# Performance work log

Hardware: AMD Instinct MI355X
Metric: run time of the kernel (lower is better)

The kernel has to match this reference:

```python
import jax, jax.numpy as jnp
import numpy as np

LN_EPS = 1e-5


def conv2d(x, w, b, stride, pad):
    # x: NCHW, w: OIHW
    y = jax.lax.conv_general_dilated(
        x, w, (stride, stride), [(pad, pad), (pad, pad)],
        dimension_numbers=("NCHW", "OIHW", "NCHW"))
    return y + b[None, :, None, None]


def gdn(x, gamma, beta):
    # y_c = x_c / sqrt(beta_c + sum_j gamma_cj * x_j^2)  (1x1 conv on x^2)
    norm = jnp.einsum("bchw,dc->bdhw", x * x, gamma) + beta[None, :, None, None]
    return x / jnp.sqrt(norm)


def layernorm(x, w, b):
    mu = jnp.mean(x, axis=-1, keepdims=True)
    var = jnp.var(x, axis=-1, keepdims=True)
    return (x - mu) / jnp.sqrt(var + LN_EPS) * w + b


def setup_inputs() -> dict:
    key = jax.random.key(0)
    ks = jax.random.split(key, 16)
    r = lambda i, shape: (jax.random.normal(ks[i], shape) * 0.02).astype(jnp.float32)
    N, M, K, D = 128, 192, 192, 128
    return {
        "x_p": jax.random.normal(ks[0], (4, 16, 3, 64, 64), jnp.float32),
        "y_g": jax.random.normal(ks[1], (64, K, 32), jnp.float32),
        "conv1_w": r(2, (N, 3, 5, 5)), "conv1_b": jnp.zeros((N,), jnp.float32),
        "gamma1": (0.1 * jnp.eye(N) + 1e-3).astype(jnp.float32), "beta1": jnp.ones((N,), jnp.float32),
        "conv2_w": r(3, (N, N, 5, 5)), "conv2_b": jnp.zeros((N,), jnp.float32),
        "gamma2": (0.1 * jnp.eye(N) + 1e-3).astype(jnp.float32), "beta2": jnp.ones((N,), jnp.float32),
        "conv3_w": r(4, (M, N, 3, 3)), "conv3_b": jnp.zeros((M,), jnp.float32),
        "ln_q_w": jnp.ones((M,), jnp.float32), "ln_q_b": jnp.zeros((M,), jnp.float32),
        "ln_kv_w": jnp.ones((K,), jnp.float32), "ln_kv_b": jnp.zeros((K,), jnp.float32),
        "ln_out_w": jnp.ones((M,), jnp.float32), "ln_out_b": jnp.zeros((M,), jnp.float32),
        "Wq": r(5, (D, M)), "Wk": r(6, (D, K)), "v_w": r(7, (1, D)),
        "Wv": r(8, (M, K)), "out_w": r(9, (M, M)), "out_b": jnp.zeros((M,), jnp.float32),
    }


def reference(x_p, y_g, conv1_w, conv1_b, gamma1, beta1, conv2_w, conv2_b,
              gamma2, beta2, conv3_w, conv3_b, ln_q_w, ln_q_b, ln_kv_w, ln_kv_b,
              ln_out_w, ln_out_b, Wq, Wk, v_w, Wv, out_w, out_b):
    B, P, C, Hp, Wp = x_p.shape
    x = x_p.reshape(B * P, C, Hp, Wp)
    # local encoder: conv s2 -> GDN -> conv s2 -> GDN -> conv s1 k3
    x = gdn(conv2d(x, conv1_w, conv1_b, 2, 2), gamma1, beta1)
    x = gdn(conv2d(x, conv2_w, conv2_b, 2, 2), gamma2, beta2)
    y_local = conv2d(x, conv3_w, conv3_b, 1, 1)          # (BP, M, h, w)
    BP, M, h, w = y_local.shape
    q = y_local.reshape(BP, M, h * w).transpose(0, 2, 1)  # (BP, Tq, M)
    kv = y_g.reshape(BP, y_g.shape[1], -1).transpose(0, 2, 1)  # (BP, Tk, K)
    q = layernorm(q, ln_q_w, ln_q_b)
    kv = layernorm(kv, ln_kv_w, ln_kv_b)
    # Bahdanau additive attention
    q_proj = jnp.einsum("bqm,dm->bqd", q, Wq)            # (BP, Tq, D)
    k_proj = jnp.einsum("bkc,dc->bkd", kv, Wk)           # (BP, Tk, D)
    energy = jnp.einsum("bqkd,d->bqk",
                        jnp.tanh(q_proj[:, :, None, :] + k_proj[:, None, :, :]),
                        v_w[0])                           # (BP, Tq, Tk)
    alpha = jax.nn.softmax(energy, axis=-1)
    v_proj = jnp.einsum("bkc,mc->bkm", kv, Wv)           # (BP, Tk, M)
    context = jnp.einsum("bqk,bkm->bqm", alpha, v_proj)
    context = jnp.einsum("bqm,nm->bqn", context, out_w) + out_b
    fused = layernorm(q + context, ln_out_w, ln_out_b)
    return fused.transpose(0, 2, 1).reshape(BP, M, h, w)
```

## Files before the change

kernel.cpp:

```cpp
#include <hip/hip_runtime.h>
#include <cstddef>
#include <cstdint>


typedef __bf16 bf16x8 __attribute__((ext_vector_type(8)));
typedef float floatx4 __attribute__((ext_vector_type(4)));
typedef unsigned short ushortT;
typedef unsigned short ushort8v __attribute__((ext_vector_type(8)));

#if __has_builtin(__builtin_amdgcn_exp2f)
#define EXP2F(x) __builtin_amdgcn_exp2f(x)
#else
#define EXP2F(x) exp2f(x)
#endif
#if __has_builtin(__builtin_amdgcn_rcpf)
#define RCPF(x) __builtin_amdgcn_rcpf(x)
#else
#define RCPF(x) (1.f / (x))
#endif

__device__ __forceinline__ ushortT f2bf(float f) {
  unsigned u = __builtin_bit_cast(unsigned, f);
  unsigned r = (u + 0x7FFFu + ((u >> 16) & 1u)) >> 16;
  return (ushortT)r;
}
__device__ __forceinline__ float bf2f(ushortT u) {
  return __builtin_bit_cast(float, ((unsigned)u) << 16);
}

static constexpr size_t OFF_T1BF = 0;
static constexpr size_t OFF_X2BF = 4194304;
static constexpr size_t OFF_T2BF = 8388608;
static constexpr size_t OFF_X3BF = 9437184;
static constexpr size_t OFF_QRAW = 10485760;
static constexpr size_t OFF_QLNB = 16777216;
static constexpr size_t OFF_KVB  = 18350080;
static constexpr size_t OFF_QP   = 18546688;
static constexpr size_t OFF_KP   = 20643840;
static constexpr size_t OFF_VP   = 20905984;
static constexpr size_t OFF_WBQ  = 21299200;
static constexpr size_t OFF_WBK  = 21311488;
static constexpr size_t OFF_WBV  = 21323776;
static constexpr size_t OFF_WBO  = 21342208;
static constexpr size_t OFF_CTXB = 21360640;
static constexpr size_t OFF_WT2  = 26079232;
static constexpr size_t OFF_WT3  = 26284032;
static constexpr size_t OFF_WC1  = 26394624;
static constexpr size_t OFF_GB1  = 26406912;
static constexpr size_t OFF_GB2  = 26415104;

__device__ __constant__ int d_TWI2[4][9] = {{ 0, 2, 4,10,12,14,20,22,24},
                                            { 1, 3,11,13,21,23, 0, 0, 0},
                                            { 5, 7, 9,15,17,19, 0, 0, 0},
                                            { 6, 8,16,18, 0, 0, 0, 0, 0}};
__device__ __constant__ int d_NT2[4] = {9, 6, 6, 4};

__device__ void dev_convw3(const float* w, ushortT* wt, int mode, int total,
                           int idx) {
  if (idx >= total) return;
  int j    = idx & 7;
  int om   = (idx >> 3) & 63;
  int kg   = (idx >> 9) & 3;
  int slab = idx >> 11;
  int mt, s, tap, T;
  if (mode == 0) {
    int ph;
    if (slab < 72) ph = 0; else if (slab < 120) ph = 1;
    else if (slab < 168) ph = 2; else ph = 3;
    const int st[4] = {0, 72, 120, 168};
    const int ns[4] = {36, 24, 24, 16};
    int rel = slab - st[ph];
    mt = rel / ns[ph]; s = rel % ns[ph];
    tap = d_TWI2[ph][s >> 2]; T = 25;
  } else {
    mt = slab / 36; s = slab % 36; tap = s >> 2; T = 9;
  }
  int cc = s & 3;
  int c  = cc * 32 + kg * 8 + j;
  int oc = mt * 64 + om;
  wt[idx] = f2bf(w[(size_t)(oc * 128 + c) * T + tap]);
}

__device__ void dev_convw1(const float* w, ushortT* wt, int idx) {
  if (idx >= 20480) return;
  int k    = idx & 31;
  int oc   = (idx >> 5) & 127;
  int slab = idx >> 12;
  int ph, i;
  if (slab < 2) { ph = 0; i = slab; } else { ph = slab - 1; i = 0; }
  int kg = k >> 3, jj = k & 7;
  int tidx = i * 8 + jj;
  float val = 0.f;
  if (kg < 3 && tidx < d_NT2[ph]) {
    int tap = d_TWI2[ph][tidx];
    val = w[(size_t)(oc * 3 + kg) * 25 + tap];
  }
  wt[idx] = f2bf(val);
}

__device__ void dev_wcast(const float* w, ushortT* wb, int total, float scale,
                          int idx) {
  if (idx < total) wb[idx] = f2bf(w[idx] * scale);
}

__global__ __launch_bounds__(256) void prep_kernel(
    const float* __restrict__ conv2_w, ushortT* __restrict__ wt2,
    const float* __restrict__ conv3_w, ushortT* __restrict__ wt3,
    const float* __restrict__ conv1_w, ushortT* __restrict__ wc1,
    const float* __restrict__ Wq, ushortT* __restrict__ wbq,
    const float* __restrict__ Wk, ushortT* __restrict__ wbk,
    const float* __restrict__ Wv, ushortT* __restrict__ wbv,
    const float* __restrict__ out_w, ushortT* __restrict__ wbo,
    const float* __restrict__ gamma1, ushortT* __restrict__ gb1,
    const float* __restrict__ gamma2, ushortT* __restrict__ gb2) {
  constexpr float C2LE = 2.88539008177792681f;
  int blk = blockIdx.x, tid = threadIdx.x;
  if (blk < 1600)      dev_convw3(conv2_w, wt2, 0, 409600, blk * 256 + tid);
  else if (blk < 2464) dev_convw3(conv3_w, wt3, 1, 221184, (blk - 1600) * 256 + tid);
  else if (blk < 2544) dev_convw1(conv1_w, wc1, (blk - 2464) * 256 + tid);
  else if (blk < 2640) dev_wcast(Wq, wbq, 24576, C2LE, (blk - 2544) * 256 + tid);
  else if (blk < 2736) dev_wcast(Wk, wbk, 24576, C2LE, (blk - 2640) * 256 + tid);
  else if (blk < 2880) dev_wcast(Wv, wbv, 36864, 1.f, (blk - 2736) * 256 + tid);
  else if (blk < 3024) dev_wcast(out_w, wbo, 36864, 1.f, (blk - 2880) * 256 + tid);
  else if (blk < 3088) dev_wcast(gamma1, gb1, 16384, 1.f, (blk - 3024) * 256 + tid);
  else                 dev_wcast(gamma2, gb2, 16384, 1.f, (blk - 3088) * 256 + tid);
}

__global__ __launch_bounds__(256, 1) void conv1_mfma_kernel(
    const float* __restrict__ x, const ushortT* __restrict__ wc1,
    const float* __restrict__ bias, ushortT* __restrict__ outb) {
  int b  = blockIdx.x >> 2;
  int yg = blockIdx.x & 3;
  int y0 = yg * 8;

  int wave = threadIdx.x >> 6;
  int lane = threadIdx.x & 63;
  int ln15 = lane & 15;
  int kg   = lane >> 4;
  int tid  = threadIdx.x;

  __shared__ ushortT simg[4680];
  __shared__ ushortT sA[5 * 128 * 40];

  for (int j = tid; j < 2340; j += 256) ((unsigned*)simg)[j] = 0u;
  __syncthreads();

  int ihBase = 2 * y0 - 2;
  const float* xb = x + (size_t)b * 3 * 4096;
  for (int j = tid; j < 960; j += 256) {
    int q = j & 15;
    int rr = j >> 4;
    int c = rr / 20, ihl = rr % 20;
    int ih = ihBase + ihl;
    if (ih >= 0 && ih < 64) {
      float4 v = *(const float4*)&xb[c * 4096 + ih * 64 + q * 4];
      int pr = ih & 1, u = ih >> 1;
      int lr = u - y0 + 1;
      int base0 = ((pr * 2 + 0) * 3 + c) * 360 + lr * 36;
      int base1 = ((pr * 2 + 1) * 3 + c) * 360 + lr * 36;
      simg[base0 + 2 * q + 1] = f2bf(v.x);
      simg[base1 + 2 * q + 1] = f2bf(v.y);
      simg[base0 + 2 * q + 2] = f2bf(v.z);
      simg[base1 + 2 * q + 2] = f2bf(v.w);
    }
  }
  for (int j = tid; j < 2560; j += 256) {
    int chunk = j & 3, row = j >> 2;
    uint4 v = *(const uint4*)&wc1[row * 32 + chunk * 8];
    *(uint4*)&sA[row * 40 + chunk * 8] = v;
  }
  __syncthreads();

  constexpr int TDR[4][9] = {{-1,-1,-1, 0, 0, 0, 1, 1, 1},
                             {-1,-1, 0, 0, 1, 1, 0, 0, 0},
                             {-1,-1,-1, 0, 0, 0, 0, 0, 0},
                             {-1,-1, 0, 0, 0, 0, 0, 0, 0}};
  constexpr int TDC[4][9] = {{-1, 0, 1,-1, 0, 1,-1, 0, 1},
                             {-1, 0,-1, 0,-1, 0, 0, 0, 0},
                             {-1, 0, 1,-1, 0, 1, 0, 0, 0},
                             {-1, 0,-1, 0, 0, 0, 0, 0, 0}};
  constexpr int NT[4]  = {9, 6, 6, 4};
  constexpr int NM[4]  = {2, 1, 1, 1};
  constexpr int SB[4]  = {0, 2, 3, 4};

  ushort8v Bf[4][5];
  #pragma unroll
  for (int ntl = 0; ntl < 4; ++ntl) {
    int ntg = wave * 4 + ntl;
    int yloc = ntg >> 1;
    int xx = (ntg & 1) * 16 + ln15;
    int lbase = (yloc + 1) * 36 + xx + 1 + kg * 360;
    #pragma unroll
    for (int ph = 0; ph < 4; ++ph) {
      int pbase = ph * 1080 + lbase;
      #pragma unroll
      for (int i = 0; i < 2; ++i) {
        if (i < NM[ph]) {
          ushort8v bv;
          #pragma unroll
          for (int j = 0; j < 8; ++j) {
            int tidx = i * 8 + j;
            if (tidx >= NT[ph]) tidx = 0;
            int off = TDR[ph][tidx] * 36 + TDC[ph][tidx];
            bv[j] = simg[pbase + off];
          }
          Bf[ntl][SB[ph] + i] = bv;
        }
      }
    }
  }

  #pragma unroll
  for (int m = 0; m < 8; ++m) {
    bf16x8 Af[5];
    #pragma unroll
    for (int s = 0; s < 5; ++s)
      Af[s] = *(const bf16x8*)&sA[(s * 128 + m * 16 + ln15) * 40 + kg * 8];
    int oc0 = m * 16 + kg * 4;
    float4 bv = *(const float4*)&bias[oc0];
    #pragma unroll
    for (int ntl = 0; ntl < 4; ++ntl) {
      floatx4 acc = (floatx4)0.f;
      #pragma unroll
      for (int s = 0; s < 5; ++s)
        acc = __builtin_amdgcn_mfma_f32_16x16x32_bf16(
            Af[s], __builtin_bit_cast(bf16x8, Bf[ntl][s]), acc, 0, 0, 0);
      int ntg = wave * 4 + ntl;
      int y = y0 + (ntg >> 1);
      int xx = (ntg & 1) * 16 + ln15;
      int p = y * 32 + xx;
      ushort4 o4 = {f2bf(acc[0] + bv.x), f2bf(acc[1] + bv.y),
                    f2bf(acc[2] + bv.z), f2bf(acc[3] + bv.w)};
      *(ushort4*)&outb[((size_t)b * 1024 + p) * 128 + oc0] = o4;
    }
  }
}

__global__ __launch_bounds__(256) void gdn_mfma_kernel(
    const ushortT* __restrict__ xbf, const ushortT* __restrict__ gb,
    const float* __restrict__ beta, ushortT* __restrict__ ybf,
    int HW, int nPixTiles, int isSplit) {
  int pt = blockIdx.x % nPixTiles;
  int b  = blockIdx.x / nPixTiles;
  int px0 = pt * 64;
  int tid = threadIdx.x;
  int wave = tid >> 6, lane = tid & 63, ln15 = lane & 15, kg = lane >> 4;

  __shared__ ushortT sG[128 * 136];
  __shared__ ushortT sX[64 * 136];

  for (int j = tid; j < 2048; j += 256) {
    int row = j >> 4, ch = j & 15;
    *(uint4*)&sG[row * 136 + ch * 8] = *(const uint4*)&gb[row * 128 + ch * 8];
  }
  for (int j = tid; j < 1024; j += 256) {
    int row = j >> 4, ch = j & 15;
    ushort8v xv = *(const ushort8v*)&xbf[((size_t)(b * HW + px0 + row)) * 128 + ch * 8];
    ushort8v sq;
    #pragma unroll
    for (int r = 0; r < 8; ++r) {
      float f = bf2f(xv[r]);
      sq[r] = f2bf(f * f);
    }
    *(ushort8v*)&sX[row * 136 + ch * 8] = sq;
  }
  __syncthreads();

  floatx4 acc[2][4];
  #pragma unroll
  for (int mi = 0; mi < 2; ++mi)
    #pragma unroll
    for (int nt = 0; nt < 4; ++nt) acc[mi][nt] = (floatx4)0.f;

  #pragma unroll
  for (int k0 = 0; k0 < 128; k0 += 32) {
    bf16x8 a0 = *(const bf16x8*)&sG[(wave * 32 + ln15) * 136 + k0 + kg * 8];
    bf16x8 a1 = *(const bf16x8*)&sG[(wave * 32 + 16 + ln15) * 136 + k0 + kg * 8];
    #pragma unroll
    for (int nt = 0; nt < 4; ++nt) {
      bf16x8 bb = *(const bf16x8*)&sX[(nt * 16 + ln15) * 136 + k0 + kg * 8];
      acc[0][nt] = __builtin_amdgcn_mfma_f32_16x16x32_bf16(a0, bb, acc[0][nt], 0, 0, 0);
      acc[1][nt] = __builtin_amdgcn_mfma_f32_16x16x32_bf16(a1, bb, acc[1][nt], 0, 0, 0);
    }
  }

  #pragma unroll
  for (int mi = 0; mi < 2; ++mi) {
    int d0 = wave * 32 + mi * 16 + kg * 4;
    float4 bt = *(const float4*)&beta[d0];
    #pragma unroll
    for (int nt = 0; nt < 4; ++nt) {
      int p = px0 + nt * 16 + ln15;
      ushort4 x4 = *(const ushort4*)&xbf[((size_t)(b * HW + p)) * 128 + d0];
      ushort4 o4;
      o4.x = f2bf(bf2f(x4.x) * rsqrtf(acc[mi][nt][0] + bt.x));
      o4.y = f2bf(bf2f(x4.y) * rsqrtf(acc[mi][nt][1] + bt.y));
      o4.z = f2bf(bf2f(x4.z) * rsqrtf(acc[mi][nt][2] + bt.z));
      o4.w = f2bf(bf2f(x4.w) * rsqrtf(acc[mi][nt][3] + bt.w));
      size_t dst;
      if (isSplit) {
        int h = p >> 5, w5 = p & 31;
        int ph = ((h & 1) << 1) | (w5 & 1);
        dst = (((size_t)b * 4 + ph) * 256 + (h >> 1) * 16 + (w5 >> 1)) * 128 + d0;
      } else {
        dst = ((size_t)b * 256 + p) * 128 + d0;
      }
      *(ushort4*)&ybf[dst] = o4;
    }
  }
}

template<int MODE>
__global__ __launch_bounds__(256, 2) void conv_mfma_kernel(
    const ushortT* __restrict__ X,
    const ushortT* __restrict__ Wt,
    const float* __restrict__ bias,
    ushortT* __restrict__ outb) {
  constexpr int OC  = (MODE == 0) ? 128 : 192;
  constexpr int NMT = OC / 64;
  constexpr int NPH = (MODE == 0) ? 4 : 1;

  int b   = blockIdx.x / (NMT * 4);
  int rem = blockIdx.x % (NMT * 4);
  int mt  = rem >> 2;
  int rs  = rem & 3;
  int r0  = rs * 4;

  int wave = threadIdx.x >> 6;
  int lane = threadIdx.x & 63;
  int ln15 = lane & 15;
  int kg   = lane >> 4;

  __shared__ ushortT simg[6 * 18 * 136];

  floatx4 acc[4];
  #pragma unroll
  for (int m = 0; m < 4; ++m) acc[m] = (floatx4)0.f;

  constexpr int NS2[4]      = {36, 24, 24, 16};
  constexpr int PHSTART2[4] = {0, 72, 120, 168};
  constexpr int TDR_2[4][9] = {{-1,-1,-1, 0, 0, 0, 1, 1, 1},
                               {-1,-1, 0, 0, 1, 1, 0, 0, 0},
                               {-1,-1,-1, 0, 0, 0, 0, 0, 0},
                               {-1,-1, 0, 0, 0, 0, 0, 0, 0}};
  constexpr int TDC_2[4][9] = {{-1, 0, 1,-1, 0, 1,-1, 0, 1},
                               {-1, 0,-1, 0,-1, 0, 0, 0, 0},
                               {-1, 0, 1,-1, 0, 1, 0, 0, 0},
                               {-1, 0,-1, 0, 0, 0, 0, 0, 0}};
  constexpr int TDR_3[9] = {-1,-1,-1, 0, 0, 0, 1, 1, 1};
  constexpr int TDC_3[9] = {-1, 0, 1,-1, 0, 1,-1, 0, 1};

  const int aoff = kg * 512 + ln15 * 8;
  uint4 apf[8][4];

  #pragma unroll
  for (int ph = 0; ph < NPH; ++ph) {
    const int NS = (MODE == 0) ? NS2[ph] : 36;
    const int slabBase = (MODE == 0) ? (PHSTART2[ph] + mt * NS2[ph]) : (mt * 36);
    const ushortT* wp0 = Wt + (size_t)slabBase * 2048 + aoff;

    __syncthreads();
    const ushortT* Xb = X + (((size_t)b * NPH + ph) * 256) * 128;
    for (int idx = threadIdx.x; idx < 1728; idx += 256) {
      int chunk = idx & 15;
      int pix = idx >> 4;
      int row = pix / 18, colm = pix - row * 18;
      int i = r0 - 1 + row, j = colm - 1;
      uint4 v = {0u, 0u, 0u, 0u};
      if (i >= 0 && i < 16 && j >= 0 && j < 16)
        v = *(const uint4*)(Xb + ((size_t)(i * 16 + j)) * 128 + chunk * 8);
      *(uint4*)&simg[(row * 18 + colm) * 136 + chunk * 8] = v;
    }
    #pragma unroll
    for (int jj = 0; jj < 8; ++jj)
      if (jj < NS) {
        #pragma unroll
        for (int m = 0; m < 4; ++m)
          apf[jj][m] = *(const uint4*)(wp0 + (size_t)jj * 2048 + m * 128);
      }
    __syncthreads();

    #pragma unroll
    for (int s0 = 0; s0 < NS; s0 += 8) {
      #pragma unroll
      for (int jj = 0; jj < 8; ++jj) {
        int s = s0 + jj;
        if (s < NS) {
          bf16x8 acur[4];
          #pragma unroll
          for (int m = 0; m < 4; ++m) acur[m] = __builtin_bit_cast(bf16x8, apf[jj][m]);
          int sp = s + 8;
          if (sp < NS) {
            #pragma unroll
            for (int m = 0; m < 4; ++m)
              apf[jj][m] = *(const uint4*)(wp0 + (size_t)sp * 2048 + m * 128);
          }
          int t  = s >> 2;
          int c0 = (s & 3) * 32;
          int dr = (MODE == 0) ? TDR_2[ph][t] : TDR_3[t];
          int dc = (MODE == 0) ? TDC_2[ph][t] : TDC_3[t];
          int lrow = wave + dr + 1;
          int lcol = ln15 + dc + 1;
          bf16x8 bfr = *(const bf16x8*)&simg[(lrow * 18 + lcol) * 136 + c0 + kg * 8];
          #pragma unroll
          for (int m = 0; m < 4; ++m)
            acc[m] = __builtin_amdgcn_mfma_f32_16x16x32_bf16(acur[m], bfr, acc[m], 0, 0, 0);
        }
      }
    }
  }

  #pragma unroll
  for (int m = 0; m < 4; ++m) {
    int mg = mt * 64 + m * 16 + kg * 4;
    float4 bv = *(const float4*)&bias[mg];
    int r = r0 + wave;
    int p = r * 16 + ln15;
    ushort4 o4 = {f2bf(acc[m][0] + bv.x), f2bf(acc[m][1] + bv.y),
                  f2bf(acc[m][2] + bv.z), f2bf(acc[m][3] + bv.w)};
    *(ushort4*)&outb[((size_t)b * 256 + p) * OC + mg] = o4;
  }
}

__device__ __forceinline__ void gemm_body(
    const ushortT* A, const ushortT* Bm, ushortT* C,
    int N, int r0, int n0, int tid) {
  __shared__ ushortT sA[128 * 196];
  __shared__ ushortT sB[64 * 196];
  for (int j = tid; j < 3072; j += 256) {
    int row = j / 24, ch = j % 24;
    *(ushort8v*)&sA[row * 196 + ch * 8] = *(const ushort8v*)&A[(size_t)(r0 + row) * 192 + ch * 8];
  }
  for (int j = tid; j < 1536; j += 256) {
    int row = j / 24, ch = j % 24;
    *(ushort8v*)&sB[row * 196 + ch * 8] = *(const ushort8v*)&Bm[(size_t)(n0 + row) * 192 + ch * 8];
  }
  __syncthreads();
  int wave = tid >> 6, lane = tid & 63, ln15 = lane & 15, kg = lane >> 4;
  floatx4 acc[2][4];
  #pragma unroll
  for (int m = 0; m < 2; ++m)
    #pragma unroll
    for (int n = 0; n < 4; ++n) acc[m][n] = (floatx4)0.f;

  #pragma unroll
  for (int k0 = 0; k0 < 192; k0 += 32) {
    bf16x8 afr[2];
    #pragma unroll
    for (int m = 0; m < 2; ++m)
      afr[m] = *(const bf16x8*)&sA[(wave * 32 + m * 16 + ln15) * 196 + k0 + kg * 8];
    #pragma unroll
    for (int n = 0; n < 4; ++n) {
      bf16x8 bfr = *(const bf16x8*)&sB[(n * 16 + ln15) * 196 + k0 + kg * 8];
      acc[0][n] = __builtin_amdgcn_mfma_f32_16x16x32_bf16(afr[0], bfr, acc[0][n], 0, 0, 0);
      acc[1][n] = __builtin_amdgcn_mfma_f32_16x16x32_bf16(afr[1], bfr, acc[1][n], 0, 0, 0);
    }
  }
  #pragma unroll
  for (int n = 0; n < 4; ++n) {
    int col = n0 + n * 16 + ln15;
    #pragma unroll
    for (int m = 0; m < 2; ++m) {
      int rowb = r0 + wave * 32 + m * 16 + kg * 4;
      #pragma unroll
      for (int r = 0; r < 4; ++r)
        C[(size_t)(rowb + r) * N + col] = f2bf(acc[m][n][r]);
    }
  }
}

__global__ __launch_bounds__(256) void gemm_qkv_kernel(
    const ushortT* __restrict__ qlnb, const ushortT* __restrict__ kvb,
    const ushortT* __restrict__ wbq, const ushortT* __restrict__ wbk,
    const ushortT* __restrict__ wbv,
    ushortT* __restrict__ qpb, ushortT* __restrict__ kpb,
    ushortT* __restrict__ vpb) {
  int blk = blockIdx.x, tid = threadIdx.x;
  if (blk < 256) {
    gemm_body(qlnb, wbq, qpb, 128, (blk >> 1) * 128, (blk & 1) * 64, tid);
  } else if (blk < 288) {
    int k = blk - 256;
    gemm_body(kvb, wbk, kpb, 128, (k >> 1) * 128, (k & 1) * 64, tid);
  } else {
    int k = blk - 288;
    gemm_body(kvb, wbv, vpb, 192, (k / 3) * 128, (k % 3) * 64, tid);
  }
}

__global__ __launch_bounds__(256) void ln_all_kernel(
    const ushortT* __restrict__ qrawb, const float* __restrict__ qw,
    const float* __restrict__ qb, ushortT* __restrict__ qlnb,
    const float* __restrict__ yg, const float* __restrict__ kw,
    const float* __restrict__ kb, ushortT* __restrict__ kvb) {
  int lane = threadIdx.x & 63;
  if (blockIdx.x < 4096) {
    int row = blockIdx.x * 4 + (threadIdx.x >> 6);
    const ushortT* xr = qrawb + (size_t)row * 192;
    float v0 = bf2f(xr[lane]), v1 = bf2f(xr[lane + 64]), v2 = bf2f(xr[lane + 128]);
    float s = v0 + v1 + v2;
    float s2 = v0 * v0 + v1 * v1 + v2 * v2;
    #pragma unroll
    for (int off = 32; off; off >>= 1) { s += __shfl_xor(s, off); s2 += __shfl_xor(s2, off); }
    float mean = s * (1.f / 192.f);
    float var = s2 * (1.f / 192.f) - mean * mean;
    float inv = rsqrtf(var + 1e-5f);
    ushortT* ybr = qlnb + (size_t)row * 192;
    ybr[lane]       = f2bf((v0 - mean) * inv * qw[lane]       + qb[lane]);
    ybr[lane + 64]  = f2bf((v1 - mean) * inv * qw[lane + 64]  + qb[lane + 64]);
    ybr[lane + 128] = f2bf((v2 - mean) * inv * qw[lane + 128] + qb[lane + 128]);
  } else {
    int row = (blockIdx.x - 4096) * 4 + (threadIdx.x >> 6);
    int b = row >> 5, t = row & 31;
    const float* src = yg + (size_t)b * 6144 + t;
    float v0 = src[(size_t)lane * 32];
    float v1 = src[(size_t)(lane + 64) * 32];
    float v2 = src[(size_t)(lane + 128) * 32];
    float s = v0 + v1 + v2;
    float s2 = v0 * v0 + v1 * v1 + v2 * v2;
    #pragma unroll
    for (int off = 32; off; off >>= 1) { s += __shfl_xor(s, off); s2 += __shfl_xor(s2, off); }
    float mean = s * (1.f / 192.f);
    float var = s2 * (1.f / 192.f) - mean * mean;
    float inv = rsqrtf(var + 1e-5f);
    ushortT* yr = kvb + (size_t)row * 192;
    yr[lane]       = f2bf((v0 - mean) * inv * kw[lane]       + kb[lane]);
    yr[lane + 64]  = f2bf((v1 - mean) * inv * kw[lane + 64]  + kb[lane + 64]);
    yr[lane + 128] = f2bf((v2 - mean) * inv * kw[lane + 128] + kb[lane + 128]);
  }
}

__global__ __launch_bounds__(256) void attn_kernel(
    const ushortT* __restrict__ qpb, const ushortT* __restrict__ kpb,
    const ushortT* __restrict__ vpb, const float* __restrict__ vw,
    ushortT* __restrict__ ctxb) {
  int b = blockIdx.x >> 4;
  int q0 = (blockIdx.x & 15) * 16;
  __shared__ float skp[32 * 132];
  __shared__ float sqp[16 * 132];
  __shared__ float svp[32 * 192];
  __shared__ float se[16][33];
  __shared__ float swm[128];
  __shared__ float sS0;
  int tid = threadIdx.x;

  for (int j = tid; j < 512; j += 256) {
    int k = j >> 4, d8 = j & 15;
    ushort8v v = *(const ushort8v*)&kpb[((size_t)(b * 32 + k)) * 128 + d8 * 8];
    #pragma unroll
    for (int r = 0; r < 8; ++r) skp[k * 132 + d8 * 8 + r] = bf2f(v[r]);
  }
  for (int j = tid; j < 256; j += 256) {
    int qq = j >> 4, d8 = j & 15;
    ushort8v v = *(const ushort8v*)&qpb[((size_t)(b * 256 + q0 + qq)) * 128 + d8 * 8];
    #pragma unroll
    for (int r = 0; r < 8; ++r) sqp[qq * 132 + d8 * 8 + r] = bf2f(v[r]);
  }
  for (int j = tid; j < 768; j += 256) {
    int k = j / 24, c8 = j % 24;
    ushort8v v = *(const ushort8v*)&vpb[((size_t)(b * 32 + k)) * 192 + c8 * 8];
    #pragma unroll
    for (int r = 0; r < 8; ++r) svp[k * 192 + c8 * 8 + r] = bf2f(v[r]);
  }
  if (tid < 128) swm[tid] = -2.f * vw[tid];
  if (tid < 64) {
    float s = vw[tid] + vw[tid + 64];
    #pragma unroll
    for (int off = 32; off; off >>= 1) s += __shfl_xor(s, off);
    if (tid == 0) sS0 = s;
  }
  __syncthreads();

  {
    int qq = tid >> 4, kc = tid & 15;
    const float4* q4 = (const float4*)&sqp[qq * 132];
    const float4* ka = (const float4*)&skp[kc * 132];
    const float4* kb = (const float4*)&skp[(kc + 16) * 132];
    const float4* w4 = (const float4*)swm;
    float S0 = sS0;
    float acc0 = S0, acc1 = S0;
    #pragma unroll 8
    for (int dj = 0; dj < 32; ++dj) {
      float4 qv = q4[dj], k0 = ka[dj], k1 = kb[dj], wv = w4[dj];
      acc0 += wv.x * RCPF(EXP2F(qv.x + k0.x) + 1.f);
      acc0 += wv.y * RCPF(EXP2F(qv.y + k0.y) + 1.f);
      acc0 += wv.z * RCPF(EXP2F(qv.z + k0.z) + 1.f);
      acc0 += wv.w * RCPF(EXP2F(qv.w + k0.w) + 1.f);
      acc1 += wv.x * RCPF(EXP2F(qv.x + k1.x) + 1.f);
      acc1 += wv.y * RCPF(EXP2F(qv.y + k1.y) + 1.f);
      acc1 += wv.z * RCPF(EXP2F(qv.z + k1.z) + 1.f);
      acc1 += wv.w * RCPF(EXP2F(qv.w + k1.w) + 1.f);
    }
    se[qq][kc] = acc0;
    se[qq][kc + 16] = acc1;
  }
  __syncthreads();
  if (tid < 16) {
    float mx = -1e30f;
    for (int k = 0; k < 32; ++k) mx = fmaxf(mx, se[tid][k]);
    float s = 0.f;
    for (int k = 0; k < 32; ++k) { float a = __expf(se[tid][k] - mx); se[tid][k] = a; s += a; }
    float invs = 1.f / s;
    for (int k = 0; k < 32; ++k) se[tid][k] *= invs;
  }
  __syncthreads();
  for (int j = tid; j < 768; j += 256) {
    int qq = j / 48, m4 = j % 48;
    const float* al = se[qq];
    float4 a = {0.f, 0.f, 0.f, 0.f};
    #pragma unroll 8
    for (int k = 0; k < 32; ++k) {
      float wk = al[k];
      float4 v = *(const float4*)&svp[k * 192 + m4 * 4];
      a.x += wk * v.x; a.y += wk * v.y; a.z += wk * v.z; a.w += wk * v.w;
    }
    ushort4 o4 = {f2bf(a.x), f2bf(a.y), f2bf(a.z), f2bf(a.w)};
    *(ushort4*)&ctxb[((size_t)(b * 256 + q0 + qq)) * 192 + m4 * 4] = o4;
  }
}

__global__ __launch_bounds__(256) void outproj_ln_kernel(
    const ushortT* __restrict__ ctxb, const ushortT* __restrict__ wbo,
    const float* __restrict__ out_b, const ushortT* __restrict__ qlnb,
    const float* __restrict__ w, const float* __restrict__ bb,
    float* __restrict__ out) {
  int b = blockIdx.x >> 2;
  int t0 = (blockIdx.x & 3) * 64;
  __shared__ float sf[64 * 193];
  int tid = threadIdx.x;
  int wave = tid >> 6, lane = tid & 63, ln15 = lane & 15, kg = lane >> 4;

  const ushortT* Arow = ctxb + ((size_t)(b * 256 + t0)) * 192;

  #pragma unroll
  for (int nc = 0; nc < 3; ++nc) {
    floatx4 acc[4];
    #pragma unroll
    for (int n = 0; n < 4; ++n) acc[n] = (floatx4)0.f;
    #pragma unroll
    for (int k0 = 0; k0 < 192; k0 += 32) {
      bf16x8 afr = *(const bf16x8*)&Arow[((size_t)(wave * 16 + ln15)) * 192 + k0 + kg * 8];
      #pragma unroll
      for (int n = 0; n < 4; ++n) {
        bf16x8 bfr = *(const bf16x8*)&wbo[((size_t)(nc * 64 + n * 16 + ln15)) * 192 + k0 + kg * 8];
        acc[n] = __builtin_amdgcn_mfma_f32_16x16x32_bf16(afr, bfr, acc[n], 0, 0, 0);
      }
    }
    #pragma unroll
    for (int n = 0; n < 4; ++n) {
      int col = nc * 64 + n * 16 + ln15;
      float bv = out_b[col];
      #pragma unroll
      for (int r = 0; r < 4; ++r)
        sf[(wave * 16 + kg * 4 + r) * 193 + col] = acc[n][r] + bv;
    }
  }
  __syncthreads();

  for (int rr = wave; rr < 64; rr += 4) {
    size_t gb = ((size_t)(b * 256 + t0 + rr)) * 192;
    float v0 = sf[rr * 193 + lane]       + bf2f(qlnb[gb + lane]);
    float v1 = sf[rr * 193 + lane + 64]  + bf2f(qlnb[gb + lane + 64]);
    float v2 = sf[rr * 193 + lane + 128] + bf2f(qlnb[gb + lane + 128]);
    float s = v0 + v1 + v2;
    float s2 = v0 * v0 + v1 * v1 + v2 * v2;
    #pragma unroll
    for (int off = 32; off; off >>= 1) { s += __shfl_xor(s, off); s2 += __shfl_xor(s2, off); }
    float mean = s * (1.f / 192.f);
    float var = s2 * (1.f / 192.f) - mean * mean;
    float inv = rsqrtf(var + 1e-5f);
    sf[rr * 193 + lane]       = (v0 - mean) * inv * w[lane]       + bb[lane];
    sf[rr * 193 + lane + 64]  = (v1 - mean) * inv * w[lane + 64]  + bb[lane + 64];
    sf[rr * 193 + lane + 128] = (v2 - mean) * inv * w[lane + 128] + bb[lane + 128];
  }
  __syncthreads();

  for (int j = tid; j < 192 * 16; j += 256) {
    int m = j >> 4, t4 = j & 15;
    float4 o4;
    o4.x = sf[(t4 * 4 + 0) * 193 + m];
    o4.y = sf[(t4 * 4 + 1) * 193 + m];
    o4.z = sf[(t4 * 4 + 2) * 193 + m];
    o4.w = sf[(t4 * 4 + 3) * 193 + m];
    *(float4*)&out[((size_t)(b * 192 + m)) * 256 + t0 + t4 * 4] = o4;
  }
}

extern "C" void kernel_launch(void* const* d_in, const int* in_sizes, int n_in,
                              void* d_out, int out_size, void* d_ws, size_t ws_size,
                              hipStream_t stream) {
  (void)in_sizes; (void)n_in; (void)out_size; (void)ws_size;
  const float* x_p     = (const float*)d_in[0];
  const float* y_g     = (const float*)d_in[1];
  const float* conv1_w = (const float*)d_in[2];
  const float* conv1_b = (const float*)d_in[3];
  const float* gamma1  = (const float*)d_in[4];
  const float* beta1   = (const float*)d_in[5];
  const float* conv2_w = (const float*)d_in[6];
  const float* conv2_b = (const float*)d_in[7];
  const float* gamma2  = (const float*)d_in[8];
  const float* beta2   = (const float*)d_in[9];
  const float* conv3_w = (const float*)d_in[10];
  const float* conv3_b = (const float*)d_in[11];
  const float* ln_q_w  = (const float*)d_in[12];
  const float* ln_q_b  = (const float*)d_in[13];
  const float* ln_kv_w = (const float*)d_in[14];
  const float* ln_kv_b = (const float*)d_in[15];
  const float* ln_out_w= (const float*)d_in[16];
  const float* ln_out_b= (const float*)d_in[17];
  const float* Wq      = (const float*)d_in[18];
  const float* Wk      = (const float*)d_in[19];
  const float* v_w     = (const float*)d_in[20];
  const float* Wv      = (const float*)d_in[21];
  const float* out_w   = (const float*)d_in[22];
  const float* out_b   = (const float*)d_in[23];
  float* out = (float*)d_out;
  float* ws  = (float*)d_ws;

  ushortT* t1bf  = (ushortT*)(ws + OFF_T1BF);
  ushortT* x2bf  = (ushortT*)(ws + OFF_X2BF);
  ushortT* t2bf  = (ushortT*)(ws + OFF_T2BF);
  ushortT* x3bf  = (ushortT*)(ws + OFF_X3BF);
  ushortT* qrawb = (ushortT*)(ws + OFF_QRAW);
  ushortT* qlnb  = (ushortT*)(ws + OFF_QLNB);
  ushortT* kvb   = (ushortT*)(ws + OFF_KVB);
  ushortT* qpb   = (ushortT*)(ws + OFF_QP);
  ushortT* kpb   = (ushortT*)(ws + OFF_KP);
  ushortT* vpb   = (ushortT*)(ws + OFF_VP);
  ushortT* wbq   = (ushortT*)(ws + OFF_WBQ);
  ushortT* wbk   = (ushortT*)(ws + OFF_WBK);
  ushortT* wbv   = (ushortT*)(ws + OFF_WBV);
  ushortT* wbo   = (ushortT*)(ws + OFF_WBO);
  ushortT* ctxb  = (ushortT*)(ws + OFF_CTXB);
  ushortT* wt2   = (ushortT*)(ws + OFF_WT2);
  ushortT* wt3   = (ushortT*)(ws + OFF_WT3);
  ushortT* wc1   = (ushortT*)(ws + OFF_WC1);
  ushortT* gb1   = (ushortT*)(ws + OFF_GB1);
  ushortT* gb2   = (ushortT*)(ws + OFF_GB2);

  prep_kernel<<<3152, 256, 0, stream>>>(conv2_w, wt2, conv3_w, wt3, conv1_w, wc1,
                                        Wq, wbq, Wk, wbk, Wv, wbv, out_w, wbo,
                                        gamma1, gb1, gamma2, gb2);
  conv1_mfma_kernel<<<256, 256, 0, stream>>>(x_p, wc1, conv1_b, t1bf);
  gdn_mfma_kernel<<<1024, 256, 0, stream>>>(t1bf, gb1, beta1, x2bf, 1024, 16, 1);
  conv_mfma_kernel<0><<<512, 256, 0, stream>>>(x2bf, wt2, conv2_b, t2bf);
  gdn_mfma_kernel<<<256, 256, 0, stream>>>(t2bf, gb2, beta2, x3bf, 256, 4, 0);
  conv_mfma_kernel<1><<<768, 256, 0, stream>>>(x3bf, wt3, conv3_b, qrawb);
  ln_all_kernel<<<4608, 256, 0, stream>>>(qrawb, ln_q_w, ln_q_b, qlnb,
                                          y_g, ln_kv_w, ln_kv_b, kvb);
  gemm_qkv_kernel<<<336, 256, 0, stream>>>(qlnb, kvb, wbq, wbk, wbv,
                                           qpb, kpb, vpb);
  attn_kernel<<<1024, 256, 0, stream>>>(qpb, kpb, vpb, v_w, ctxb);
  outproj_ln_kernel<<<256, 256, 0, stream>>>(ctxb, wbo, out_b, qlnb,
                                             ln_out_w, ln_out_b, out);
}
```

Measured before the change: 264.1 us.

## Fuse LayerNorm, QKV projections, attention and output projection into one kernel

Merges four kernels (LN, QKV GEMM, additive attention, outproj+LN) into one per-(batch, 64-token) block kernel that keeps intermediates in shared memory. This removes the global-memory round trips for qln, kv, q/k/v projections and context, plus three launches. The cost is that K/V LN and projections are recomputed by each of the 4 blocks per batch, and only 256 blocks run with large LDS use. The attention energy loop now reads bf16 from LDS instead of fp32, and the q LayerNorm is recomputed at the residual step.

```diff
diff --git a/kernel.cpp b/kernel.cpp
--- a/kernel.cpp
+++ b/kernel.cpp
@@ -33,16 +33,10 @@
 static constexpr size_t OFF_T2BF = 8388608;
 static constexpr size_t OFF_X3BF = 9437184;
 static constexpr size_t OFF_QRAW = 10485760;
-static constexpr size_t OFF_QLNB = 16777216;
-static constexpr size_t OFF_KVB  = 18350080;
-static constexpr size_t OFF_QP   = 18546688;
-static constexpr size_t OFF_KP   = 20643840;
-static constexpr size_t OFF_VP   = 20905984;
 static constexpr size_t OFF_WBQ  = 21299200;
 static constexpr size_t OFF_WBK  = 21311488;
 static constexpr size_t OFF_WBV  = 21323776;
 static constexpr size_t OFF_WBO  = 21342208;
-static constexpr size_t OFF_CTXB = 21360640;
 static constexpr size_t OFF_WT2  = 26079232;
 static constexpr size_t OFF_WT3  = 26284032;
 static constexpr size_t OFF_WC1  = 26394624;
@@ -422,80 +416,37 @@
   }
 }
 
-__device__ __forceinline__ void gemm_body(
-    const ushortT* A, const ushortT* Bm, ushortT* C,
-    int N, int r0, int n0, int tid) {
-  __shared__ ushortT sA[128 * 196];
-  __shared__ ushortT sB[64 * 196];
-  for (int j = tid; j < 3072; j += 256) {
-    int row = j / 24, ch = j % 24;
-    *(ushort8v*)&sA[row * 196 + ch * 8] = *(const ushort8v*)&A[(size_t)(r0 + row) * 192 + ch * 8];
-  }
-  for (int j = tid; j < 1536; j += 256) {
-    int row = j / 24, ch = j % 24;
-    *(ushort8v*)&sB[row * 196 + ch * 8] = *(const ushort8v*)&Bm[(size_t)(n0 + row) * 192 + ch * 8];
-  }
-  __syncthreads();
-  int wave = tid >> 6, lane = tid & 63, ln15 = lane & 15, kg = lane >> 4;
-  floatx4 acc[2][4];
-  #pragma unroll
-  for (int m = 0; m < 2; ++m)
-    #pragma unroll
-    for (int n = 0; n < 4; ++n) acc[m][n] = (floatx4)0.f;
-
-  #pragma unroll
-  for (int k0 = 0; k0 < 192; k0 += 32) {
-    bf16x8 afr[2];
-    #pragma unroll
-    for (int m = 0; m < 2; ++m)
-      afr[m] = *(const bf16x8*)&sA[(wave * 32 + m * 16 + ln15) * 196 + k0 + kg * 8];
-    #pragma unroll
-    for (int n = 0; n < 4; ++n) {
-      bf16x8 bfr = *(const bf16x8*)&sB[(n * 16 + ln15) * 196 + k0 + kg * 8];
-      acc[0][n] = __builtin_amdgcn_mfma_f32_16x16x32_bf16(afr[0], bfr, acc[0][n], 0, 0, 0);
-      acc[1][n] = __builtin_amdgcn_mfma_f32_16x16x32_bf16(afr[1], bfr, acc[1][n], 0, 0, 0);
-    }
-  }
-  #pragma unroll
-  for (int n = 0; n < 4; ++n) {
-    int col = n0 + n * 16 + ln15;
-    #pragma unroll
-    for (int m = 0; m < 2; ++m) {
-      int rowb = r0 + wave * 32 + m * 16 + kg * 4;
-      #pragma unroll
-      for (int r = 0; r < 4; ++r)
-        C[(size_t)(rowb + r) * N + col] = f2bf(acc[m][n][r]);
-    }
-  }
-}
-
-__global__ __launch_bounds__(256) void gemm_qkv_kernel(
-    const ushortT* __restrict__ qlnb, const ushortT* __restrict__ kvb,
+__global__ __launch_bounds__(256) void attn_mega_kernel(
+    const ushortT* __restrict__ qrawb, const float* __restrict__ ln_q_w,
+    const float* __restrict__ ln_q_b, const float* __restrict__ yg,
+    const float* __restrict__ ln_kv_w, const float* __restrict__ ln_kv_b,
     const ushortT* __restrict__ wbq, const ushortT* __restrict__ wbk,
-    const ushortT* __restrict__ wbv,
-    ushortT* __restrict__ qpb, ushortT* __restrict__ kpb,
-    ushortT* __restrict__ vpb) {
-  int blk = blockIdx.x, tid = threadIdx.x;
-  if (blk < 256) {
-    gemm_body(qlnb, wbq, qpb, 128, (blk >> 1) * 128, (blk & 1) * 64, tid);
-  } else if (blk < 288) {
-    int k = blk - 256;
-    gemm_body(kvb, wbk, kpb, 128, (k >> 1) * 128, (k & 1) * 64, tid);
-  } else {
-    int k = blk - 288;
-    gemm_body(kvb, wbv, vpb, 192, (k / 3) * 128, (k % 3) * 64, tid);
-  }
-}
-
-__global__ __launch_bounds__(256) void ln_all_kernel(
-    const ushortT* __restrict__ qrawb, const float* __restrict__ qw,
-    const float* __restrict__ qb, ushortT* __restrict__ qlnb,
-    const float* __restrict__ yg, const float* __restrict__ kw,
-    const float* __restrict__ kb, ushortT* __restrict__ kvb) {
-  int lane = threadIdx.x & 63;
-  if (blockIdx.x < 4096) {
-    int row = blockIdx.x * 4 + (threadIdx.x >> 6);
-    const ushortT* xr = qrawb + (size_t)row * 192;
+    const ushortT* __restrict__ wbv, const ushortT* __restrict__ wbo,
+    const float* __restrict__ vw, const float* __restrict__ out_b,
+    const float* __restrict__ ln_out_w, const float* __restrict__ ln_out_b,
+    float* __restrict__ out) {
+  __shared__ ushortT smem[32256];
+  ushortT* sqln = smem;
+  ushortT* skv  = smem + 12800;
+  ushortT* sqp  = smem + 19200;
+  ushortT* skp  = smem + 27904;
+  ushortT* svp  = smem;
+  float*   se   = (float*)(smem + 6400);
+  float*   swm  = (float*)(smem + 10624);
+  float*   sS0  = (float*)(smem + 10880);
+  ushortT* sctx = smem + 19200;
+  float*   sf   = (float*)smem;
+
+  int b  = blockIdx.x >> 2;
+  int t0 = (blockIdx.x & 3) * 64;
+  int tid  = threadIdx.x;
+  int wave = tid >> 6;
+  int lane = tid & 63;
+  int ln15 = lane & 15;
+  int kg   = lane >> 4;
+
+  for (int r = wave; r < 64; r += 4) {
+    const ushortT* xr = qrawb + ((size_t)(b * 256 + t0 + r)) * 192;
     float v0 = bf2f(xr[lane]), v1 = bf2f(xr[lane + 64]), v2 = bf2f(xr[lane + 128]);
     float s = v0 + v1 + v2;
     float s2 = v0 * v0 + v1 * v1 + v2 * v2;
@@ -504,14 +455,12 @@
     float mean = s * (1.f / 192.f);
     float var = s2 * (1.f / 192.f) - mean * mean;
     float inv = rsqrtf(var + 1e-5f);
-    ushortT* ybr = qlnb + (size_t)row * 192;
-    ybr[lane]       = f2bf((v0 - mean) * inv * qw[lane]       + qb[lane]);
-    ybr[lane + 64]  = f2bf((v1 - mean) * inv * qw[lane + 64]  + qb[lane + 64]);
-    ybr[lane + 128] = f2bf((v2 - mean) * inv * qw[lane + 128] + qb[lane + 128]);
-  } else {
-    int row = (blockIdx.x - 4096) * 4 + (threadIdx.x >> 6);
-    int b = row >> 5, t = row & 31;
-    const float* src = yg + (size_t)b * 6144 + t;
+    sqln[r * 200 + lane]       = f2bf((v0 - mean) * inv * ln_q_w[lane]       + ln_q_b[lane]);
+    sqln[r * 200 + lane + 64]  = f2bf((v1 - mean) * inv * ln_q_w[lane + 64]  + ln_q_b[lane + 64]);
+    sqln[r * 200 + lane + 128] = f2bf((v2 - mean) * inv * ln_q_w[lane + 128] + ln_q_b[lane + 128]);
+  }
+  for (int r = wave; r < 32; r += 4) {
+    const float* src = yg + (size_t)b * 6144 + r;
     float v0 = src[(size_t)lane * 32];
     float v1 = src[(size_t)(lane + 64) * 32];
     float v2 = src[(size_t)(lane + 128) * 32];
@@ -522,166 +471,179 @@
     float mean = s * (1.f / 192.f);
     float var = s2 * (1.f / 192.f) - mean * mean;
     float inv = rsqrtf(var + 1e-5f);
-    ushortT* yr = kvb + (size_t)row * 192;
-    yr[lane]       = f2bf((v0 - mean) * inv * kw[lane]       + kb[lane]);
-    yr[lane + 64]  = f2bf((v1 - mean) * inv * kw[lane + 64]  + kb[lane + 64]);
-    yr[lane + 128] = f2bf((v2 - mean) * inv * kw[lane + 128] + kb[lane + 128]);
-  }
-}
-
-__global__ __launch_bounds__(256) void attn_kernel(
-    const ushortT* __restrict__ qpb, const ushortT* __restrict__ kpb,
-    const ushortT* __restrict__ vpb, const float* __restrict__ vw,
-    ushortT* __restrict__ ctxb) {
-  int b = blockIdx.x >> 4;
-  int q0 = (blockIdx.x & 15) * 16;
-  __shared__ float skp[32 * 132];
-  __shared__ float sqp[16 * 132];
-  __shared__ float svp[32 * 192];
-  __shared__ float se[16][33];
-  __shared__ float swm[128];
-  __shared__ float sS0;
-  int tid = threadIdx.x;
-
-  for (int j = tid; j < 512; j += 256) {
-    int k = j >> 4, d8 = j & 15;
-    ushort8v v = *(const ushort8v*)&kpb[((size_t)(b * 32 + k)) * 128 + d8 * 8];
-    #pragma unroll
-    for (int r = 0; r < 8; ++r) skp[k * 132 + d8 * 8 + r] = bf2f(v[r]);
-  }
-  for (int j = tid; j < 256; j += 256) {
-    int qq = j >> 4, d8 = j & 15;
-    ushort8v v = *(const ushort8v*)&qpb[((size_t)(b * 256 + q0 + qq)) * 128 + d8 * 8];
-    #pragma unroll
-    for (int r = 0; r < 8; ++r) sqp[qq * 132 + d8 * 8 + r] = bf2f(v[r]);
-  }
-  for (int j = tid; j < 768; j += 256) {
-    int k = j / 24, c8 = j % 24;
-    ushort8v v = *(const ushort8v*)&vpb[((size_t)(b * 32 + k)) * 192 + c8 * 8];
-    #pragma unroll
-    for (int r = 0; r < 8; ++r) svp[k * 192 + c8 * 8 + r] = bf2f(v[r]);
+    skv[r * 200 + lane]       = f2bf((v0 - mean) * inv * ln_kv_w[lane]       + ln_kv_b[lane]);
+    skv[r * 200 + lane + 64]  = f2bf((v1 - mean) * inv * ln_kv_w[lane + 64]  + ln_kv_b[lane + 64]);
+    skv[r * 200 + lane + 128] = f2bf((v2 - mean) * inv * ln_kv_w[lane + 128] + ln_kv_b[lane + 128]);
+  }
+  __syncthreads();
+
+  for (int ti = wave; ti < 32; ti += 4) {
+    int rt = ti >> 3, ct = ti & 7;
+    floatx4 acc = (floatx4)0.f;
+    #pragma unroll
+    for (int k0 = 0; k0 < 192; k0 += 32) {
+      bf16x8 afr = *(const bf16x8*)&sqln[(rt * 16 + ln15) * 200 + k0 + kg * 8];
+      bf16x8 bfr = *(const bf16x8*)&wbq[((size_t)(ct * 16 + ln15)) * 192 + k0 + kg * 8];
+      acc = __builtin_amdgcn_mfma_f32_16x16x32_bf16(afr, bfr, acc, 0, 0, 0);
+    }
+    #pragma unroll
+    for (int r = 0; r < 4; ++r)
+      sqp[(rt * 16 + kg * 4 + r) * 136 + ct * 16 + ln15] = f2bf(acc[r]);
+  }
+  for (int ti = wave; ti < 16; ti += 4) {
+    int rt = ti >> 3, ct = ti & 7;
+    floatx4 acc = (floatx4)0.f;
+    #pragma unroll
+    for (int k0 = 0; k0 < 192; k0 += 32) {
+      bf16x8 afr = *(const bf16x8*)&skv[(rt * 16 + ln15) * 200 + k0 + kg * 8];
+      bf16x8 bfr = *(const bf16x8*)&wbk[((size_t)(ct * 16 + ln15)) * 192 + k0 + kg * 8];
+      acc = __builtin_amdgcn_mfma_f32_16x16x32_bf16(afr, bfr, acc, 0, 0, 0);
+    }
+    #pragma unroll
+    for (int r = 0; r < 4; ++r)
+      skp[(rt * 16 + kg * 4 + r) * 136 + ct * 16 + ln15] = f2bf(acc[r]);
+  }
+  __syncthreads();
+
+  for (int ti = wave; ti < 24; ti += 4) {
+    int rt = ti / 12, ct = ti % 12;
+    floatx4 acc = (floatx4)0.f;
+    #pragma unroll
+    for (int k0 = 0; k0 < 192; k0 += 32) {
+      bf16x8 afr = *(const bf16x8*)&skv[(rt * 16 + ln15) * 200 + k0 + kg * 8];
+      bf16x8 bfr = *(const bf16x8*)&wbv[((size_t)(ct * 16 + ln15)) * 192 + k0 + kg * 8];
+      acc = __builtin_amdgcn_mfma_f32_16x16x32_bf16(afr, bfr, acc, 0, 0, 0);
+    }
+    #pragma unroll
+    for (int r = 0; r < 4; ++r)
+      svp[(rt * 16 + kg * 4 + r) * 200 + ct * 16 + ln15] = f2bf(acc[r]);
   }
   if (tid < 128) swm[tid] = -2.f * vw[tid];
   if (tid < 64) {
     float s = vw[tid] + vw[tid + 64];
     #pragma unroll
     for (int off = 32; off; off >>= 1) s += __shfl_xor(s, off);
-    if (tid == 0) sS0 = s;
+    if (tid == 0) *sS0 = s;
   }
   __syncthreads();
 
   {
-    int qq = tid >> 4, kc = tid & 15;
-    const float4* q4 = (const float4*)&sqp[qq * 132];
-    const float4* ka = (const float4*)&skp[kc * 132];
-    const float4* kb = (const float4*)&skp[(kc + 16) * 132];
+    float S0v = *sS0;
+    int qq0 = tid >> 4, kc = tid & 15;
     const float4* w4 = (const float4*)swm;
-    float S0 = sS0;
-    float acc0 = S0, acc1 = S0;
-    #pragma unroll 8
-    for (int dj = 0; dj < 32; ++dj) {
-      float4 qv = q4[dj], k0 = ka[dj], k1 = kb[dj], wv = w4[dj];
-      acc0 += wv.x * RCPF(EXP2F(qv.x + k0.x) + 1.f);
-      acc0 += wv.y * RCPF(EXP2F(qv.y + k0.y) + 1.f);
-      acc0 += wv.z * RCPF(EXP2F(qv.z + k0.z) + 1.f);
-      acc0 += wv.w * RCPF(EXP2F(qv.w + k0.w) + 1.f);
-      acc1 += wv.x * RCPF(EXP2F(qv.x + k1.x) + 1.f);
-      acc1 += wv.y * RCPF(EXP2F(qv.y + k1.y) + 1.f);
-      acc1 += wv.z * RCPF(EXP2F(qv.z + k1.z) + 1.f);
-      acc1 += wv.w * RCPF(EXP2F(qv.w + k1.w) + 1.f);
-    }
-    se[qq][kc] = acc0;
-    se[qq][kc + 16] = acc1;
-  }
-  __syncthreads();
-  if (tid < 16) {
+    #pragma unroll
+    for (int st = 0; st < 4; ++st) {
+      int qq = st * 16 + qq0;
+      const ushortT* qrow = sqp + qq * 136;
+      const ushortT* kr0 = skp + kc * 136;
+      const ushortT* kr1 = skp + (kc + 16) * 136;
+      float acc0 = S0v, acc1 = S0v;
+      #pragma unroll 8
+      for (int d4 = 0; d4 < 32; ++d4) {
+        ushort4 qu = *(const ushort4*)&qrow[d4 * 4];
+        ushort4 k0u = *(const ushort4*)&kr0[d4 * 4];
+        ushort4 k1u = *(const ushort4*)&kr1[d4 * 4];
+        float4 wv = w4[d4];
+        float qx = bf2f(qu.x), qy = bf2f(qu.y), qz = bf2f(qu.z), qw = bf2f(qu.w);
+        acc0 += wv.x * RCPF(EXP2F(qx + bf2f(k0u.x)) + 1.f);
+        acc0 += wv.y * RCPF(EXP2F(qy + bf2f(k0u.y)) + 1.f);
+        acc0 += wv.z * RCPF(EXP2F(qz + bf2f(k0u.z)) + 1.f);
+        acc0 += wv.w * RCPF(EXP2F(qw + bf2f(k0u.w)) + 1.f);
+        acc1 += wv.x * RCPF(EXP2F(qx + bf2f(k1u.x)) + 1.f);
+        acc1 += wv.y * RCPF(EXP2F(qy + bf2f(k1u.y)) + 1.f);
+        acc1 += wv.z * RCPF(EXP2F(qz + bf2f(k1u.z)) + 1.f);
+        acc1 += wv.w * RCPF(EXP2F(qw + bf2f(k1u.w)) + 1.f);
+      }
+      se[qq * 33 + kc] = acc0;
+      se[qq * 33 + kc + 16] = acc1;
+    }
+  }
+  __syncthreads();
+
+  if (tid < 64) {
+    float* ser = se + tid * 33;
     float mx = -1e30f;
-    for (int k = 0; k < 32; ++k) mx = fmaxf(mx, se[tid][k]);
+    for (int k = 0; k < 32; ++k) mx = fmaxf(mx, ser[k]);
     float s = 0.f;
-    for (int k = 0; k < 32; ++k) { float a = __expf(se[tid][k] - mx); se[tid][k] = a; s += a; }
+    for (int k = 0; k < 32; ++k) { float a = __expf(ser[k] - mx); ser[k] = a; s += a; }
     float invs = 1.f / s;
-    for (int k = 0; k < 32; ++k) se[tid][k] *= invs;
-  }
-  __syncthreads();
-  for (int j = tid; j < 768; j += 256) {
+    for (int k = 0; k < 32; ++k) ser[k] *= invs;
+  }
+  __syncthreads();
+
+  for (int j = tid; j < 3072; j += 256) {
     int qq = j / 48, m4 = j % 48;
-    const float* al = se[qq];
+    const float* al = se + qq * 33;
     float4 a = {0.f, 0.f, 0.f, 0.f};
     #pragma unroll 8
     for (int k = 0; k < 32; ++k) {
       float wk = al[k];
-      float4 v = *(const float4*)&svp[k * 192 + m4 * 4];
-      a.x += wk * v.x; a.y += wk * v.y; a.z += wk * v.z; a.w += wk * v.w;
+      ushort4 vv = *(const ushort4*)&svp[k * 200 + m4 * 4];
+      a.x += wk * bf2f(vv.x); a.y += wk * bf2f(vv.y);
+      a.z += wk * bf2f(vv.z); a.w += wk * bf2f(vv.w);
     }
     ushort4 o4 = {f2bf(a.x), f2bf(a.y), f2bf(a.z), f2bf(a.w)};
-    *(ushort4*)&ctxb[((size_t)(b * 256 + q0 + qq)) * 192 + m4 * 4] = o4;
-  }
-}
-
-__global__ __launch_bounds__(256) void outproj_ln_kernel(
-    const ushortT* __restrict__ ctxb, const ushortT* __restrict__ wbo,
-    const float* __restrict__ out_b, const ushortT* __restrict__ qlnb,
-    const float* __restrict__ w, const float* __restrict__ bb,
-    float* __restrict__ out) {
-  int b = blockIdx.x >> 2;
-  int t0 = (blockIdx.x & 3) * 64;
-  __shared__ float sf[64 * 193];
-  int tid = threadIdx.x;
-  int wave = tid >> 6, lane = tid & 63, ln15 = lane & 15, kg = lane >> 4;
-
-  const ushortT* Arow = ctxb + ((size_t)(b * 256 + t0)) * 192;
-
-  #pragma unroll
-  for (int nc = 0; nc < 3; ++nc) {
-    floatx4 acc[4];
-    #pragma unroll
-    for (int n = 0; n < 4; ++n) acc[n] = (floatx4)0.f;
-    #pragma unroll
-    for (int k0 = 0; k0 < 192; k0 += 32) {
-      bf16x8 afr = *(const bf16x8*)&Arow[((size_t)(wave * 16 + ln15)) * 192 + k0 + kg * 8];
+    *(ushort4*)&sctx[qq * 200 + m4 * 4] = o4;
+  }
+  __syncthreads();
+
+  for (int hh = 0; hh < 2; ++hh) {
+    for (int ti = wave; ti < 24; ti += 4) {
+      int rt = ti / 12, ct = ti % 12;
+      floatx4 acc = (floatx4)0.f;
       #pragma unroll
-      for (int n = 0; n < 4; ++n) {
-        bf16x8 bfr = *(const bf16x8*)&wbo[((size_t)(nc * 64 + n * 16 + ln15)) * 192 + k0 + kg * 8];
-        acc[n] = __builtin_amdgcn_mfma_f32_16x16x32_bf16(afr, bfr, acc[n], 0, 0, 0);
+      for (int k0 = 0; k0 < 192; k0 += 32) {
+        bf16x8 afr = *(const bf16x8*)&sctx[(hh * 32 + rt * 16 + ln15) * 200 + k0 + kg * 8];
+        bf16x8 bfr = *(const bf16x8*)&wbo[((size_t)(ct * 16 + ln15)) * 192 + k0 + kg * 8];
+        acc = __builtin_amdgcn_mfma_f32_16x16x32_bf16(afr, bfr, acc, 0, 0, 0);
       }
-    }
-    #pragma unroll
-    for (int n = 0; n < 4; ++n) {
-      int col = nc * 64 + n * 16 + ln15;
-      float bv = out_b[col];
+      float bv = out_b[ct * 16 + ln15];
       #pragma unroll
       for (int r = 0; r < 4; ++r)
-        sf[(wave * 16 + kg * 4 + r) * 193 + col] = acc[n][r] + bv;
-    }
-  }
-  __syncthreads();
-
-  for (int rr = wave; rr < 64; rr += 4) {
-    size_t gb = ((size_t)(b * 256 + t0 + rr)) * 192;
-    float v0 = sf[rr * 193 + lane]       + bf2f(qlnb[gb + lane]);
-    float v1 = sf[rr * 193 + lane + 64]  + bf2f(qlnb[gb + lane + 64]);
-    float v2 = sf[rr * 193 + lane + 128] + bf2f(qlnb[gb + lane + 128]);
-    float s = v0 + v1 + v2;
-    float s2 = v0 * v0 + v1 * v1 + v2 * v2;
-    #pragma unroll
-    for (int off = 32; off; off >>= 1) { s += __shfl_xor(s, off); s2 += __shfl_xor(s2, off); }
-    float mean = s * (1.f / 192.f);
-    float var = s2 * (1.f / 192.f) - mean * mean;
-    float inv = rsqrtf(var + 1e-5f);
-    sf[rr * 193 + lane]       = (v0 - mean) * inv * w[lane]       + bb[lane];
-    sf[rr * 193 + lane + 64]  = (v1 - mean) * inv * w[lane + 64]  + bb[lane + 64];
-    sf[rr * 193 + lane + 128] = (v2 - mean) * inv * w[lane + 128] + bb[lane + 128];
-  }
-  __syncthreads();
-
-  for (int j = tid; j < 192 * 16; j += 256) {
-    int m = j >> 4, t4 = j & 15;
-    float4 o4;
-    o4.x = sf[(t4 * 4 + 0) * 193 + m];
-    o4.y = sf[(t4 * 4 + 1) * 193 + m];
-    o4.z = sf[(t4 * 4 + 2) * 193 + m];
-    o4.w = sf[(t4 * 4 + 3) * 193 + m];
-    *(float4*)&out[((size_t)(b * 192 + m)) * 256 + t0 + t4 * 4] = o4;
+        sf[(rt * 16 + kg * 4 + r) * 193 + ct * 16 + ln15] = acc[r] + bv;
+    }
+    __syncthreads();
+
+    for (int rr = wave; rr < 32; rr += 4) {
+      int t = t0 + hh * 32 + rr;
+      const ushortT* xr = qrawb + ((size_t)(b * 256 + t)) * 192;
+      float r0_ = bf2f(xr[lane]), r1_ = bf2f(xr[lane + 64]), r2_ = bf2f(xr[lane + 128]);
+      float s = r0_ + r1_ + r2_;
+      float s2 = r0_ * r0_ + r1_ * r1_ + r2_ * r2_;
+      #pragma unroll
+      for (int off = 32; off; off >>= 1) { s += __shfl_xor(s, off); s2 += __shfl_xor(s2, off); }
+      float mean = s * (1.f / 192.f);
+      float var = s2 * (1.f / 192.f) - mean * mean;
+      float inv = rsqrtf(var + 1e-5f);
+      float q0 = (r0_ - mean) * inv * ln_q_w[lane]       + ln_q_b[lane];
+      float q1 = (r1_ - mean) * inv * ln_q_w[lane + 64]  + ln_q_b[lane + 64];
+      float q2 = (r2_ - mean) * inv * ln_q_w[lane + 128] + ln_q_b[lane + 128];
+      float v0 = sf[rr * 193 + lane]       + q0;
+      float v1 = sf[rr * 193 + lane + 64]  + q1;
+      float v2 = sf[rr * 193 + lane + 128] + q2;
+      float t_s = v0 + v1 + v2;
+      float t_s2 = v0 * v0 + v1 * v1 + v2 * v2;
+      #pragma unroll
+      for (int off = 32; off; off >>= 1) { t_s += __shfl_xor(t_s, off); t_s2 += __shfl_xor(t_s2, off); }
+      float m2 = t_s * (1.f / 192.f);
+      float var2 = t_s2 * (1.f / 192.f) - m2 * m2;
+      float inv2 = rsqrtf(var2 + 1e-5f);
+      sf[rr * 193 + lane]       = (v0 - m2) * inv2 * ln_out_w[lane]       + ln_out_b[lane];
+      sf[rr * 193 + lane + 64]  = (v1 - m2) * inv2 * ln_out_w[lane + 64]  + ln_out_b[lane + 64];
+      sf[rr * 193 + lane + 128] = (v2 - m2) * inv2 * ln_out_w[lane + 128] + ln_out_b[lane + 128];
+    }
+    __syncthreads();
+
+    for (int j = tid; j < 1536; j += 256) {
+      int m = j >> 3, t4 = j & 7;
+      float4 o4;
+      o4.x = sf[(t4 * 4 + 0) * 193 + m];
+      o4.y = sf[(t4 * 4 + 1) * 193 + m];
+      o4.z = sf[(t4 * 4 + 2) * 193 + m];
+      o4.w = sf[(t4 * 4 + 3) * 193 + m];
+      *(float4*)&out[((size_t)(b * 192 + m)) * 256 + t0 + hh * 32 + t4 * 4] = o4;
+    }
+    __syncthreads();
   }
 }
 
@@ -721,16 +683,10 @@
   ushortT* t2bf  = (ushortT*)(ws + OFF_T2BF);
   ushortT* x3bf  = (ushortT*)(ws + OFF_X3BF);
   ushortT* qrawb = (ushortT*)(ws + OFF_QRAW);
-  ushortT* qlnb  = (ushortT*)(ws + OFF_QLNB);
-  ushortT* kvb   = (ushortT*)(ws + OFF_KVB);
-  ushortT* qpb   = (ushortT*)(ws + OFF_QP);
-  ushortT* kpb   = (ushortT*)(ws + OFF_KP);
-  ushortT* vpb   = (ushortT*)(ws + OFF_VP);
   ushortT* wbq   = (ushortT*)(ws + OFF_WBQ);
   ushortT* wbk   = (ushortT*)(ws + OFF_WBK);
   ushortT* wbv   = (ushortT*)(ws + OFF_WBV);
   ushortT* wbo   = (ushortT*)(ws + OFF_WBO);
-  ushortT* ctxb  = (ushortT*)(ws + OFF_CTXB);
   ushortT* wt2   = (ushortT*)(ws + OFF_WT2);
   ushortT* wt3   = (ushortT*)(ws + OFF_WT3);
   ushortT* wc1   = (ushortT*)(ws + OFF_WC1);
@@ -745,11 +701,8 @@
   conv_mfma_kernel<0><<<512, 256, 0, stream>>>(x2bf, wt2, conv2_b, t2bf);
   gdn_mfma_kernel<<<256, 256, 0, stream>>>(t2bf, gb2, beta2, x3bf, 256, 4, 0);
   conv_mfma_kernel<1><<<768, 256, 0, stream>>>(x3bf, wt3, conv3_b, qrawb);
-  ln_all_kernel<<<4608, 256, 0, stream>>>(qrawb, ln_q_w, ln_q_b, qlnb,
-                                          y_g, ln_kv_w, ln_kv_b, kvb);
-  gemm_qkv_kernel<<<336, 256, 0, stream>>>(qlnb, kvb, wbq, wbk, wbv,
-                                           qpb, kpb, vpb);
-  attn_kernel<<<1024, 256, 0, stream>>>(qpb, kpb, vpb, v_w, ctxb);
-  outproj_ln_kernel<<<256, 256, 0, stream>>>(ctxb, wbo, out_b, qlnb,
-                                             ln_out_w, ln_out_b, out);
-}
+  attn_mega_kernel<<<256, 256, 0, stream>>>(qrawb, ln_q_w, ln_q_b, y_g,
+                                            ln_kv_w, ln_kv_b, wbq, wbk, wbv,
+                                            wbo, v_w, out_b, ln_out_w,
+                                            ln_out_b, out);
+}
```

After: 267.6 us. About the same (+1.3%).
